# Optimization experiments

Hardware: AMD Instinct MI355X
Metric: run time of the kernel (lower is better)

Reference implementation:

```python
import jax, jax.numpy as jnp
import numpy as np

B, L, H, LAB = 64, 128, 512, 128

def setup_inputs() -> dict:
    key = jax.random.key(0)
    ks = jax.random.split(key, 8)
    s = 1.0 / np.sqrt(H)  # PyTorch LSTM/Linear uniform bound as a std-ish scale
    return {
        "x": jax.random.normal(ks[0], (B, L, 2 * H), jnp.float32),
        "hi": jax.random.normal(ks[1], (B, L, 2 * H), jnp.float32),
        "W_ih": jax.random.normal(ks[2], (4 * H, 5 * H), jnp.float32) * s,
        "W_hh": jax.random.normal(ks[3], (4 * H, H), jnp.float32) * s,
        "b_ih": jax.random.normal(ks[4], (4 * H,), jnp.float32) * s,
        "b_hh": jax.random.normal(ks[5], (4 * H,), jnp.float32) * s,
        "W_fc": jax.random.normal(ks[6], (LAB, H), jnp.float32) * s,
        "b_fc": jax.random.normal(ks[7], (LAB,), jnp.float32) * s,
    }

def _cell(xi, h, c, W_ih, W_hh, b_ih, b_hh):
    # PyTorch LSTMCell math, gate order: input, forget, cell(g), output
    gates = xi @ W_ih.T + b_ih + h @ W_hh.T + b_hh  # [4H]
    i, f, g, o = jnp.split(gates, 4)
    i = jax.nn.sigmoid(i); f = jax.nn.sigmoid(f); o = jax.nn.sigmoid(o)
    g = jnp.tanh(g)
    c = f * c + i * g
    h = o * jnp.tanh(c)
    return h, c

def reference(x, hi, W_ih, W_hh, b_ih, b_hh, W_fc, b_fc):
    Bm, Lm, _ = x.shape
    Hm = W_hh.shape[1]
    xs = jnp.concatenate([x, hi], axis=-1).transpose(1, 0, 2)  # [L, B, 4H]
    # Faithful to the torch code: nn.LSTM (batch_first=False) is fed [B,1,5H]
    # with state (1,1,H), so it scans the batch dim as 'time' with a single
    # shared (h,c) that also persists across outer timesteps.
    def time_step(carry, x_t):
        h, c, prev_out = carry  # h,c: [H]; prev_out: [B,H] (outputs of prev t)
        inp = jnp.concatenate([x_t, prev_out], axis=-1)  # [B, 5H]
        def batch_step(hc, xi):
            hh, cc = hc
            hh, cc = _cell(xi, hh, cc, W_ih, W_hh, b_ih, b_hh)
            return (hh, cc), hh
        (h, c), outs = jax.lax.scan(batch_step, (h, c), inp)  # outs: [B,H]
        return (h, c, outs), outs
    init = (jnp.zeros((Hm,), x.dtype), jnp.zeros((Hm,), x.dtype),
            jnp.zeros((Bm, Hm), x.dtype))
    _, all_out = jax.lax.scan(time_step, init, xs)  # [L, B, H]
    output = all_out.transpose(1, 0, 2)  # [B, L, H]
    return output @ W_fc.T + b_fc  # [B, L, label_size]
```

## Files before the change

### kernel.cpp

```cpp
#include <hip/hip_runtime.h>
#include <stdint.h>


#define HDIM   512
#define NSTEP  8192
#define XDIM   2048
#define IN5H   2560
#define LSEQ   128
#define LAB    128
#define SPIN_LIMIT 65536

typedef float f32x4 __attribute__((ext_vector_type(4)));
typedef short bf16x8 __attribute__((ext_vector_type(8)));

__device__ __forceinline__ unsigned f2bf(float v){
  unsigned u = __float_as_uint(v);
  u += 0x7fffu + ((u >> 16) & 1u);
  return u >> 16;
}
__device__ __forceinline__ float bfu(unsigned half16){
  return __uint_as_float(half16 << 16);
}
template<int CTRL>
__device__ __forceinline__ float dpp_add(float x){
  const int yi = __builtin_amdgcn_update_dpp(0, __float_as_int(x), CTRL, 0xF, 0xF, true);
  return x + __int_as_float(yi);
}
__device__ __forceinline__ float wave_reduce63(float x){
  x = dpp_add<0x111>(x);
  x = dpp_add<0x112>(x);
  x = dpp_add<0x114>(x);
  x = dpp_add<0x118>(x);
  x = dpp_add<0x142>(x);
  x = dpp_add<0x143>(x);
  return x;
}

__global__ __launch_bounds__(256) void gemm_pre(
    const float* __restrict__ x, const float* __restrict__ hi,
    const float* __restrict__ Wih, const float* __restrict__ bih,
    const float* __restrict__ bhh, unsigned* __restrict__ pre32)
{
  __shared__ unsigned short As[128][40];
  __shared__ unsigned short Bs[128][40];
  const int tid = threadIdx.x;
  const int bm = blockIdx.x, bn = blockIdx.y;
  const int lane = tid & 63, wv = tid >> 6;
  const int wm = wv & 1, wn = wv >> 1;

  const int srow = tid >> 1;
  const int ch   = (tid & 1) * 16;

  const int gr = bm*128 + srow;
  const int bb = gr & 63, tt = gr >> 6;
  const float* ax = x  + (size_t)(bb*LSEQ + tt) * 1024;
  const float* ah = hi + (size_t)(bb*LSEQ + tt) * 1024;
  const int R = bn*128 + srow;
  const float* bw = Wih + (size_t)R * IN5H;

  f32x4 acc[4][4];
  #pragma unroll
  for (int m=0;m<4;++m)
    #pragma unroll
    for (int n=0;n<4;++n) acc[m][n] = (f32x4){0.f,0.f,0.f,0.f};

  for (int kc = 0; kc < XDIM; kc += 32){
    const int c0 = kc + ch;
    const float* ap = (c0 < 1024) ? (ax + c0) : (ah + (c0 - 1024));
    #pragma unroll
    for (int q=0;q<4;++q){
      float4 va = *(const float4*)(ap + 4*q);
      float4 vb = *(const float4*)(bw + c0 + 4*q);
      ushort4 ua; ua.x=f2bf(va.x); ua.y=f2bf(va.y); ua.z=f2bf(va.z); ua.w=f2bf(va.w);
      ushort4 ub; ub.x=f2bf(vb.x); ub.y=f2bf(vb.y); ub.z=f2bf(vb.z); ub.w=f2bf(vb.w);
      *(ushort4*)&As[srow][ch + 4*q] = ua;
      *(ushort4*)&Bs[srow][ch + 4*q] = ub;
    }
    __syncthreads();
    bf16x8 afr[4], bfr[4];
    const int mr = wm*64 + (lane & 15);
    const int nr = wn*64 + (lane & 15);
    const int ko = (lane >> 4) * 8;
    #pragma unroll
    for (int m=0;m<4;++m) afr[m] = *(const bf16x8*)&As[mr + 16*m][ko];
    #pragma unroll
    for (int n=0;n<4;++n) bfr[n] = *(const bf16x8*)&Bs[nr + 16*n][ko];
    #pragma unroll
    for (int m=0;m<4;++m)
      #pragma unroll
      for (int n=0;n<4;++n)
        acc[m][n] = __builtin_amdgcn_mfma_f32_16x16x32_bf16(afr[m], bfr[n], acc[m][n], 0, 0, 0);
    __syncthreads();
  }
  #pragma unroll
  for (int n=0;n<4;++n){
    const int scol = bn*128 + wn*64 + 16*n + (lane & 15);
    const float bias = bih[scol] + bhh[scol];
    #pragma unroll
    for (int m=0;m<4;++m){
      const int sr0 = bm*128 + wm*64 + 16*m + (lane >> 4)*4;
      #pragma unroll
      for (int q=0;q<4;++q){
        const float v = acc[m][n][q] + bias;
        const float vn = __shfl_xor(v, 1, 64);
        if (!(lane & 1)){
          const unsigned word = f2bf(v) | (f2bf(vn) << 16);
          pre32[(size_t)(sr0 + q) * 1024 + (scol >> 1)] = word;
        }
      }
    }
  }
}

__global__ __launch_bounds__(256)
__attribute__((amdgpu_waves_per_eu(1,1)))
void lstm_seq(
    const float* __restrict__ Wih, const float* __restrict__ Whh,
    const unsigned* __restrict__ pre32, unsigned* __restrict__ units)
{
  const int tid = threadIdx.x;
  const int l = tid & 63;
  const int j0 = blockIdx.x * 4 + (tid >> 6);

  float wh[4][8], wu[4][8];
  #pragma unroll
  for (int g=0; g<4; ++g){
    const float* ph = Whh + (size_t)(g*HDIM + j0)*HDIM;
    const float* pu = Wih + (size_t)(g*HDIM + j0)*IN5H + XDIM;
    #pragma unroll
    for (int k=0; k<8; ++k){
      const int col = 2*l + 128*(k>>1) + (k&1);
      wh[g][k] = ph[col]; wu[g][k] = pu[col];
    }
  }
  #pragma unroll
  for (int g=0; g<4; ++g)
    #pragma unroll
    for (int k=0; k<8; ++k){
      asm volatile("" : "+v"(wh[g][k]));
      asm volatile("" : "+v"(wu[g][k]));
    }

  const int phalf = j0 >> 1, psel = j0 & 1;
  float pr[4];
  #pragma unroll
  for (int g=0; g<4; ++g){
    const unsigned w0 = pre32[(size_t)0*1024 + g*256 + phalf];
    pr[g] = psel ? bfu(w0 >> 16) : bfu(w0 & 0xffffu);
  }

  float uvc[8];
  #pragma unroll
  for (int k=0;k<8;++k) uvc[k] = 0.f;

  float cst = 0.f;
  int dead = 0;

  for (int s = 0; s < NSTEP; ++s){
    unsigned pw[4];
    const bool pf  = (s + 1 < NSTEP);
    const bool upf = (s + 1 >= 64) && pf;
    if (pf){
      #pragma unroll
      for (int g=0; g<4; ++g)
        pw[g] = pre32[(size_t)(s+1)*1024 + g*256 + phalf];
    }
    unsigned long long un[4];
    if (upf){
      const unsigned long long* bp =
          (const unsigned long long*)(units + (size_t)(s-63)*HDIM) + l;
      #pragma unroll
      for (int c=0;c<4;++c)
        un[c] = __hip_atomic_load(bp + 64*c, __ATOMIC_RELAXED, __HIP_MEMORY_SCOPE_AGENT);
    }

    float hv[8];
    if (s == 0){
      #pragma unroll
      for (int k=0;k<8;++k) hv[k] = 0.f;
    } else {
      const unsigned long long* bp =
          (const unsigned long long*)(units + (size_t)(s-1)*HDIM) + l;
      unsigned long long v[4];
      if (dead){
        #pragma unroll
        for (int c=0;c<4;++c) v[c] = __hip_atomic_load(bp + 64*c, __ATOMIC_RELAXED, __HIP_MEMORY_SCOPE_AGENT);
      } else {
        int trips = 0, ok;
        do {
          #pragma unroll
          for (int c=0;c<4;++c) v[c] = __hip_atomic_load(bp + 64*c, __ATOMIC_RELAXED, __HIP_MEMORY_SCOPE_AGENT);
          int lok = 1;
          #pragma unroll
          for (int c=0;c<4;++c){
            lok &= (((unsigned)(v[c] >> 16) & 0xffffu) == (unsigned)s);
            lok &= (((unsigned)(v[c] >> 48)) == (unsigned)s);
          }
          ok = __all(lok);
        } while (!ok && ++trips < SPIN_LIMIT);
        if (!ok) dead = 1;
      }
      #pragma unroll
      for (int c=0;c<4;++c){
        hv[2*c]   = bfu((unsigned)v[c] & 0xffffu);
        hv[2*c+1] = bfu((unsigned)(v[c] >> 32) & 0xffffu);
      }
    }

    float a0=0.f, a1=0.f, a2=0.f, a3=0.f;
    #pragma unroll
    for (int k=0;k<8;++k){
      a0 += wh[0][k]*hv[k]; a1 += wh[1][k]*hv[k];
      a2 += wh[2][k]*hv[k]; a3 += wh[3][k]*hv[k];
    }
    #pragma unroll
    for (int k=0;k<8;++k){
      a0 += wu[0][k]*uvc[k]; a1 += wu[1][k]*uvc[k];
      a2 += wu[2][k]*uvc[k]; a3 += wu[3][k]*uvc[k];
    }
    a0 = wave_reduce63(a0);
    a1 = wave_reduce63(a1);
    a2 = wave_reduce63(a2);
    a3 = wave_reduce63(a3);

    float gi = a0 + pr[0];
    float gf = a1 + pr[1];
    float gg = a2 + pr[2];
    float go = a3 + pr[3];
    gi = 1.f/(1.f + __expf(-gi));
    gf = 1.f/(1.f + __expf(-gf));
    go = 1.f/(1.f + __expf(-go));
    float e2 = __expf(2.f * fminf(fmaxf(gg, -15.f), 15.f));
    gg = (e2 - 1.f) / (e2 + 1.f);
    cst = gf*cst + gi*gg;
    float e2c = __expf(2.f * fminf(fmaxf(cst, -15.f), 15.f));
    const float hval = go * ((e2c - 1.f) / (e2c + 1.f));

    if (l == 63){
      const unsigned unit = ((unsigned)(s + 1) << 16) | f2bf(hval);
      __hip_atomic_store(units + (size_t)s*HDIM + j0, unit,
                         __ATOMIC_RELAXED, __HIP_MEMORY_SCOPE_AGENT);
    }

    if (upf){
      int lok = 1;
      #pragma unroll
      for (int c=0;c<4;++c){
        lok &= (((unsigned)(un[c] >> 16) & 0xffffu) == (unsigned)(s-62));
        lok &= (((unsigned)(un[c] >> 48)) == (unsigned)(s-62));
      }
      if (!__all(lok) && !dead){
        const unsigned long long* bp =
            (const unsigned long long*)(units + (size_t)(s-63)*HDIM) + l;
        int trips = 0, ok;
        do {
          #pragma unroll
          for (int c=0;c<4;++c)
            un[c] = __hip_atomic_load(bp + 64*c, __ATOMIC_RELAXED, __HIP_MEMORY_SCOPE_AGENT);
          int lk = 1;
          #pragma unroll
          for (int c=0;c<4;++c){
            lk &= (((unsigned)(un[c] >> 16) & 0xffffu) == (unsigned)(s-62));
            lk &= (((unsigned)(un[c] >> 48)) == (unsigned)(s-62));
          }
          ok = __all(lk);
        } while (!ok && ++trips < SPIN_LIMIT);
        if (!ok) dead = 1;
      }
      #pragma unroll
      for (int c=0;c<4;++c){
        uvc[2*c]   = bfu((unsigned)un[c] & 0xffffu);
        uvc[2*c+1] = bfu((unsigned)(un[c] >> 32) & 0xffffu);
      }
    } else {
      #pragma unroll
      for (int k=0;k<8;++k) uvc[k] = 0.f;
    }
    if (pf){
      #pragma unroll
      for (int g=0; g<4; ++g)
        pr[g] = psel ? bfu(pw[g] >> 16) : bfu(pw[g] & 0xffffu);
    }
  }
}

__global__ __launch_bounds__(256) void fc_kernel(
    const unsigned* __restrict__ units,
    const float* __restrict__ Wfc, const float* __restrict__ bfc,
    float* __restrict__ out)
{
  __shared__ float hbuf[8][512];
  const int tid = threadIdx.x;
  const int s0 = blockIdx.x * 8;
  #pragma unroll
  for (int r=0;r<16;++r){
    const int q = tid + 256*r;
    const int si = q >> 9, j = q & 511;
    hbuf[si][j] = bfu(units[(size_t)(s0 + si)*HDIM + j] & 0xffffu);
  }
  __syncthreads();
  const int lab = tid & 127, sg = tid >> 7;
  const float* wrow = Wfc + (size_t)lab * HDIM;
  const float bias = bfc[lab];
  for (int si = sg; si < 8; si += 2){
    float sum = 0.f;
    #pragma unroll 4
    for (int j=0;j<HDIM;j+=4){
      const float4 wv = *(const float4*)(wrow + j);
      sum += wv.x*hbuf[si][j] + wv.y*hbuf[si][j+1]
           + wv.z*hbuf[si][j+2] + wv.w*hbuf[si][j+3];
    }
    const int s = s0 + si;
    const int bb = s & 63, tt = s >> 6;
    out[((size_t)(bb*LSEQ + tt))*LAB + lab] = sum + bias;
  }
}

__global__ void sentinel_kernel(float* out, int n){
  const int i = blockIdx.x*256 + threadIdx.x;
  if (i < n) out[i] = 12345.0f;
}

extern "C" void kernel_launch(void* const* d_in, const int* in_sizes, int n_in,
                              void* d_out, int out_size, void* d_ws, size_t ws_size,
                              hipStream_t stream)
{
  const float* x   = (const float*)d_in[0];
  const float* hi  = (const float*)d_in[1];
  const float* Wih = (const float*)d_in[2];
  const float* Whh = (const float*)d_in[3];
  const float* bih = (const float*)d_in[4];
  const float* bhh = (const float*)d_in[5];
  const float* Wfc = (const float*)d_in[6];
  const float* bfc = (const float*)d_in[7];
  float* out = (float*)d_out;

  const size_t MB = 1024*1024;
  if (ws_size >= 48*MB){
    unsigned* pre32 = (unsigned*)d_ws;
    unsigned* units = (unsigned*)((char*)d_ws + 32*MB);
    gemm_pre<<<dim3(64, 16), 256, 0, stream>>>(x, hi, Wih, bih, bhh, pre32);
    lstm_seq<<<128, 256, 0, stream>>>(Wih, Whh, pre32, units);
    fc_kernel<<<1024, 256, 0, stream>>>(units, Wfc, bfc, out);
  } else {
    sentinel_kernel<<<(out_size + 255)/256, 256, 0, stream>>>(out, out_size);
  }
}
```

Baseline: 14.50 ms.

## Run the LSTM recurrence on a single XCD using a tagged L2 ring buffer

Adds a new recurrence kernel that elects one XCD through an atomic compare-and-swap on a control word, so that only 32 workgroups on that XCD run the 8192-step loop. Hidden state moves through a 128-slot ring buffer of bf16 values, each carrying a step tag in its upper bits. Readers spin on sc0 loads until every tag matches, which removes the need for separate flags or cross-XCD barriers and should shorten per-step latency. If a spin times out or the election fails, the original kernel still runs as a fallback, but it skips itself when the completion counter shows all waves finished. The election and counters assume the control words start at the 0xAAAAAAAA workspace fill pattern, so the fast path depends on how the harness initialises the workspace.

```diff
diff --git a/kernel.cpp b/kernel.cpp
--- a/kernel.cpp
+++ b/kernel.cpp
@@ -9,9 +9,12 @@
 #define LSEQ   128
 #define LAB    128
 #define SPIN_LIMIT 65536
+#define NXRING 128
+#define SPINX  16384
 
 typedef float f32x4 __attribute__((ext_vector_type(4)));
 typedef short bf16x8 __attribute__((ext_vector_type(8)));
+typedef unsigned u32x4 __attribute__((ext_vector_type(4)));
 
 __device__ __forceinline__ unsigned f2bf(float v){
   unsigned u = __float_as_uint(v);
@@ -34,6 +37,32 @@
   x = dpp_add<0x142>(x);
   x = dpp_add<0x143>(x);
   return x;
+}
+
+__device__ __forceinline__ void ld32_sc0(const unsigned* p, u32x4& a, u32x4& b){
+  asm volatile("global_load_dwordx4 %0, %2, off sc0\n\t"
+               "global_load_dwordx4 %1, %2, off offset:16 sc0\n\t"
+               "s_waitcnt vmcnt(0)"
+               : "=&v"(a), "=&v"(b)
+               : "v"(p)
+               : "memory");
+}
+__device__ __forceinline__ int tagok8(u32x4 a, u32x4 b, unsigned t){
+  int ok = ((a[0] >> 16) == t);
+  ok &= ((a[1] >> 16) == t);
+  ok &= ((a[2] >> 16) == t);
+  ok &= ((a[3] >> 16) == t);
+  ok &= ((b[0] >> 16) == t);
+  ok &= ((b[1] >> 16) == t);
+  ok &= ((b[2] >> 16) == t);
+  ok &= ((b[3] >> 16) == t);
+  return ok;
+}
+__device__ __forceinline__ void decode8(u32x4 a, u32x4 b, float* h){
+  h[0] = __uint_as_float(a[0] << 16); h[1] = __uint_as_float(a[1] << 16);
+  h[2] = __uint_as_float(a[2] << 16); h[3] = __uint_as_float(a[3] << 16);
+  h[4] = __uint_as_float(b[0] << 16); h[5] = __uint_as_float(b[1] << 16);
+  h[6] = __uint_as_float(b[2] << 16); h[7] = __uint_as_float(b[3] << 16);
 }
 
 __global__ __launch_bounds__(256) void gemm_pre(
@@ -114,10 +143,150 @@
 
 __global__ __launch_bounds__(256)
 __attribute__((amdgpu_waves_per_eu(1,1)))
+void lstm_seq_xcd(
+    const float* __restrict__ Wih, const float* __restrict__ Whh,
+    const unsigned* __restrict__ pre32, unsigned* __restrict__ units,
+    unsigned* __restrict__ ring, unsigned* __restrict__ ctrl)
+{
+  __shared__ int sh_part;
+  const int tid = threadIdx.x;
+  if (tid == 0){
+    const unsigned my_xcd = (unsigned)__builtin_amdgcn_s_getreg(6164) & 0xFu;
+    const unsigned tagv = 0xE1EC0000u | my_xcd;
+    const unsigned prev = atomicCAS(ctrl + 0, 0xAAAAAAAAu, tagv);
+    const unsigned chosen = (prev == 0xAAAAAAAAu) ? tagv : prev;
+    int part = -1;
+    if (chosen == tagv){
+      const unsigned r = atomicAdd(ctrl + 16, 1u) - 0xAAAAAAAAu;
+      if (r < 32u) part = (int)r;
+    }
+    sh_part = part;
+  }
+  __syncthreads();
+  const int wgr = sh_part;
+  if (wgr < 0) return;
+
+  const int l   = tid & 63;
+  const int wv  = tid >> 6;
+  const int wid = wgr*4 + wv;
+  const int j0  = wid*4;
+  const int c0  = 8*l;
+
+  f32x4 wh[4][4][2], wu[4][4][2];
+  #pragma unroll
+  for (int g=0; g<4; ++g)
+    #pragma unroll
+    for (int m=0; m<4; ++m){
+      const float* ph = Whh + (size_t)(g*HDIM + j0 + m)*HDIM + c0;
+      const float* pu = Wih + (size_t)(g*HDIM + j0 + m)*IN5H + XDIM + c0;
+      wh[g][m][0] = *(const f32x4*)ph;  wh[g][m][1] = *(const f32x4*)(ph+4);
+      wu[g][m][0] = *(const f32x4*)pu;  wu[g][m][1] = *(const f32x4*)(pu+4);
+    }
+  #pragma unroll
+  for (int g=0; g<4; ++g)
+    #pragma unroll
+    for (int m=0; m<4; ++m){
+      asm volatile("" : "+v"(wh[g][m][0]), "+v"(wh[g][m][1]));
+      asm volatile("" : "+v"(wu[g][m][0]), "+v"(wu[g][m][1]));
+    }
+
+  const int pw0 = wid*2;
+  float cst[4] = {0.f,0.f,0.f,0.f};
+  int halted = 0;
+
+  #pragma clang loop unroll(disable)
+  for (int s = 0; s < NSTEP; ++s){
+    unsigned long long pwv[4];
+    #pragma unroll
+    for (int g=0; g<4; ++g)
+      pwv[g] = __builtin_nontemporal_load(
+          (const unsigned long long*)(pre32 + (size_t)s*1024 + g*256 + pw0));
+
+    float uv[8];
+    if (s >= 64){
+      const unsigned* up = ring + (((unsigned)(s-64)) & (NXRING-1))*HDIM + c0;
+      u32x4 ua, ub;
+      ld32_sc0(up, ua, ub);
+      const unsigned utg = (unsigned)(s - 63);
+      if (!__all(tagok8(ua, ub, utg))){
+        int trips = 0, ok;
+        do { ld32_sc0(up, ua, ub); ok = __all(tagok8(ua, ub, utg)); }
+        while (!ok && ++trips < SPINX);
+        if (!ok) halted = 1;
+      }
+      decode8(ua, ub, uv);
+    } else {
+      #pragma unroll
+      for (int k=0;k<8;++k) uv[k] = 0.f;
+    }
+    if (halted) break;
+
+    float hv[8];
+    if (s == 0){
+      #pragma unroll
+      for (int k=0;k<8;++k) hv[k] = 0.f;
+    } else {
+      const unsigned* hp = ring + (((unsigned)(s-1)) & (NXRING-1))*HDIM + c0;
+      const unsigned htg = (unsigned)s;
+      u32x4 ha, hb;
+      int trips = 0, ok;
+      do { ld32_sc0(hp, ha, hb); ok = __all(tagok8(ha, hb, htg)); }
+      while (!ok && ++trips < SPINX);
+      if (!ok){ halted = 1; break; }
+      decode8(ha, hb, hv);
+    }
+
+    const f32x4 h40 = {hv[0],hv[1],hv[2],hv[3]}, h41 = {hv[4],hv[5],hv[6],hv[7]};
+    const f32x4 u40 = {uv[0],uv[1],uv[2],uv[3]}, u41 = {uv[4],uv[5],uv[6],uv[7]};
+
+    float sums[4][4];
+    #pragma unroll
+    for (int g=0; g<4; ++g)
+      #pragma unroll
+      for (int m=0; m<4; ++m){
+        f32x4 acc = wh[g][m][0]*h40 + wh[g][m][1]*h41
+                  + wu[g][m][0]*u40 + wu[g][m][1]*u41;
+        sums[g][m] = wave_reduce63(acc[0]+acc[1]+acc[2]+acc[3]);
+      }
+
+    unsigned pkt[4];
+    const unsigned tag = (unsigned)(s + 1) << 16;
+    #pragma unroll
+    for (int m=0; m<4; ++m){
+      float gi = sums[0][m] + bfu((unsigned)(pwv[0] >> (16*m)) & 0xffffu);
+      float gf = sums[1][m] + bfu((unsigned)(pwv[1] >> (16*m)) & 0xffffu);
+      float gg = sums[2][m] + bfu((unsigned)(pwv[2] >> (16*m)) & 0xffffu);
+      float go = sums[3][m] + bfu((unsigned)(pwv[3] >> (16*m)) & 0xffffu);
+      gi = 1.f/(1.f + __expf(-gi));
+      gf = 1.f/(1.f + __expf(-gf));
+      go = 1.f/(1.f + __expf(-go));
+      float e2 = __expf(2.f * fminf(fmaxf(gg, -15.f), 15.f));
+      gg = (e2 - 1.f) / (e2 + 1.f);
+      cst[m] = gf*cst[m] + gi*gg;
+      float e2c = __expf(2.f * fminf(fmaxf(cst[m], -15.f), 15.f));
+      const float hval = go * ((e2c - 1.f) / (e2c + 1.f));
+      pkt[m] = tag | f2bf(hval);
+    }
+    if (l == 63){
+      u32x4 o; o[0]=pkt[0]; o[1]=pkt[1]; o[2]=pkt[2]; o[3]=pkt[3];
+      *(u32x4*)(ring + (((unsigned)s) & (NXRING-1))*HDIM + j0) = o;
+      __builtin_nontemporal_store(o, (u32x4*)(units + (size_t)s*HDIM + j0));
+    }
+  }
+
+  if (!halted && l == 0) atomicAdd(ctrl + 32, 1u);
+}
+
+__global__ __launch_bounds__(256)
+__attribute__((amdgpu_waves_per_eu(1,1)))
 void lstm_seq(
     const float* __restrict__ Wih, const float* __restrict__ Whh,
-    const unsigned* __restrict__ pre32, unsigned* __restrict__ units)
+    const unsigned* __restrict__ pre32, unsigned* __restrict__ units,
+    const unsigned* __restrict__ done_ctrl)
 {
+  if (done_ctrl){
+    if (*(volatile const unsigned*)done_ctrl == 0xAAAAAAAAu + 128u) return;
+  }
   const int tid = threadIdx.x;
   const int l = tid & 63;
   const int j0 = blockIdx.x * 4 + (tid >> 6);
@@ -336,11 +505,20 @@
   float* out = (float*)d_out;
 
   const size_t MB = 1024*1024;
-  if (ws_size >= 48*MB){
+  if (ws_size >= 49*MB){
+    unsigned* pre32 = (unsigned*)d_ws;
+    unsigned* units = (unsigned*)((char*)d_ws + 32*MB);
+    unsigned* ring  = (unsigned*)((char*)d_ws + 48*MB);
+    unsigned* ctrl  = (unsigned*)((char*)d_ws + 48*MB + 256*1024);
+    gemm_pre<<<dim3(64, 16), 256, 0, stream>>>(x, hi, Wih, bih, bhh, pre32);
+    lstm_seq_xcd<<<512, 256, 0, stream>>>(Wih, Whh, pre32, units, ring, ctrl);
+    lstm_seq<<<128, 256, 0, stream>>>(Wih, Whh, pre32, units, ctrl + 32);
+    fc_kernel<<<1024, 256, 0, stream>>>(units, Wfc, bfc, out);
+  } else if (ws_size >= 48*MB){
     unsigned* pre32 = (unsigned*)d_ws;
     unsigned* units = (unsigned*)((char*)d_ws + 32*MB);
     gemm_pre<<<dim3(64, 16), 256, 0, stream>>>(x, hi, Wih, bih, bhh, pre32);
-    lstm_seq<<<128, 256, 0, stream>>>(Wih, Whh, pre32, units);
+    lstm_seq<<<128, 256, 0, stream>>>(Wih, Whh, pre32, units, nullptr);
     fc_kernel<<<1024, 256, 0, stream>>>(units, Wfc, bfc, out);
   } else {
     sentinel_kernel<<<(out_size + 255)/256, 256, 0, stream>>>(out, out_size);
```

Result: slower. 17.32 ms (+19.4%).
